# Kernel optimization log

Hardware: AMD Instinct MI355X
Metric: run time of the kernel (lower is better)

The kernel has to match this reference:

```python
import jax, jax.numpy as jnp
import numpy as np

B, N, D, K = 16, 1024, 512, 8
NUM_ITERS = 3
EPS = 1e-08
LN_EPS = 1e-05


def layer_norm(x, g, b):
    m = jnp.mean(x, axis=-1, keepdims=True)
    v = jnp.var(x, axis=-1, keepdims=True)
    return (x - m) * jax.lax.rsqrt(v + LN_EPS) * g + b


def setup_inputs() -> dict:
    key = jax.random.key(0)
    ks = jax.random.split(key, 8)
    s = 1.0 / np.sqrt(D)
    return {
        "embeddings": jax.random.normal(ks[0], (B, N, D), jnp.float32),
        "noise_init": jax.random.normal(ks[1], (B, K, D), jnp.float32),
        "noise_final": jax.random.normal(ks[2], (B, K, D), jnp.float32),
        "slots_mu": jax.random.normal(ks[3], (1, K, D), jnp.float32) * s,
        "slots_logsigma": jax.random.normal(ks[4], (1, K, D), jnp.float32) * s,
        "mixing_coeffs": jnp.ones((1, K), jnp.float32) / K,
        "Wk": jax.random.normal(ks[5], (D, D), jnp.float32) * s,
        "bk": jnp.zeros((D,), jnp.float32),
        "Wq": jax.random.normal(ks[6], (D, D), jnp.float32) * s,
        "bq": jnp.zeros((D,), jnp.float32),
        "Wv": jax.random.normal(ks[7], (D, D), jnp.float32) * s,
        "bv": jnp.zeros((D,), jnp.float32),
        "ln_g": jnp.ones((D,), jnp.float32),
        "ln_b": jnp.zeros((D,), jnp.float32),
    }


def reference(embeddings, noise_init, noise_final, slots_mu, slots_logsigma,
              mixing_coeffs, Wk, bk, Wq, bq, Wv, bv, ln_g, ln_b):
    b, n, d = embeddings.shape
    mixing = jnp.broadcast_to(mixing_coeffs, (b, K))           # [B,K]
    mu = jnp.broadcast_to(slots_mu, (b, K, d))                 # [B,K,D]
    sigma = jnp.exp(jnp.broadcast_to(slots_logsigma, (b, K, d)))
    slots = mu + sigma * noise_init                            # sampled slots

    x = layer_norm(embeddings, ln_g, ln_b)
    keys = x @ Wk + bk                                         # [B,N,D]
    values = x @ Wv + bv                                       # [B,N,D]
    # slots are never updated inside the loop, so queries are loop-invariant
    queries = slots @ Wq + bq                                  # [B,K,D]

    log2pi = jnp.float32(np.log(2.0 * np.pi))
    attn = None
    for _ in range(NUM_ITERS):
        diff = keys[:, :, None, :] - queries[:, None, :, :]    # [B,N,K,D]
        gll = -0.5 * jnp.sum(diff * diff / (sigma[:, None] ** 2 + EPS), axis=-1)  # [B,N,K]
        gll = (-0.5 * d * log2pi
               - 0.5 * jnp.sum(jnp.log(jnp.abs(sigma) + EPS), axis=-1)[:, None, :]
               + gll)
        attn = mixing[:, None, :] * gll                        # [B,N,K]
        attn = attn / jnp.sum(attn, axis=-1, keepdims=True)
        attn = attn / (jnp.sum(attn, axis=1, keepdims=True) + EPS)
        mu = jnp.einsum('bnk,bnd->bkd', attn, values)          # [B,K,D]
        diff2 = values[:, :, None, :] - mu[:, None, :, :]      # [B,N,K,D]
        sigma = jnp.einsum('bnk,bnkd->bkd', attn, diff2 * diff2)
        mixing = jnp.sum(attn, axis=1) / n

    sigma = jnp.maximum(jnp.abs(sigma), EPS)
    slots = mu + sigma * noise_final
    return slots, jnp.transpose(attn, (0, 2, 1))
```

## Files before the change

kernel.cpp:

```cpp
#include <hip/hip_runtime.h>
#include <math.h>

#define BB 16
#define NN 1024
#define DD 512
#define KK 8
#define EPS_ 1e-8f
#define LN_EPS_ 1e-5f
#define GLL_C0 (-470.4965290007924f)

typedef __attribute__((ext_vector_type(8))) short short8;
typedef __attribute__((ext_vector_type(4))) short short4v;
typedef __attribute__((ext_vector_type(4))) float f32x4;
typedef __attribute__((ext_vector_type(4))) int int4v;

static __device__ inline short f2bf(float f) {
    unsigned u = __builtin_bit_cast(unsigned, f);
    u = (u + 0x7fff + ((u >> 16) & 1)) >> 16;
    return (short)u;
}
static __device__ inline float bf2f(short s) {
    unsigned u = ((unsigned)(unsigned short)s) << 16;
    return __builtin_bit_cast(float, u);
}

struct Params {
    const float *emb, *noise_init, *noise_final, *slots_mu, *slots_logsg,
                *mixing_co, *Wk, *bk, *Wq, *bq, *Wv, *bv, *ln_g, *ln_b;
    float *out;
    float *queries, *attn, *s1p, *s2p, *off, *mix16, *colsum;
    short *Abf, *Kbf, *Vbf, *WtKV, *WqT, *slotbf, *F_bt;
};

__global__ __launch_bounds__(256) void k_pre(Params p)
{
    __shared__ __align__(16) short eb[4352];
    int u = blockIdx.x, tid = threadIdx.x;
    if (u < 4096) {
        int row  = u * 4 + (tid >> 6);
        int lane = tid & 63;
        const float* e = p.emb + (size_t)row * DD + lane * 8;
        float4 v0 = *(const float4*)e;
        float4 v1 = *(const float4*)(e + 4);
        float v[8] = {v0.x, v0.y, v0.z, v0.w, v1.x, v1.y, v1.z, v1.w};
        float s = 0.0f;
#pragma unroll
        for (int j = 0; j < 8; j++) s += v[j];
#pragma unroll
        for (int off = 32; off; off >>= 1) s += __shfl_xor(s, off);
        float m = s * (1.0f / DD);
        float vs = 0.0f;
#pragma unroll
        for (int j = 0; j < 8; j++) { float d = v[j] - m; vs = fmaf(d, d, vs); }
#pragma unroll
        for (int off = 32; off; off >>= 1) vs += __shfl_xor(vs, off);
        float rstd = rsqrtf(vs * (1.0f / DD) + LN_EPS_);

        float4 g0 = *(const float4*)&p.ln_g[lane * 8];
        float4 g1 = *(const float4*)&p.ln_g[lane * 8 + 4];
        float4 b0 = *(const float4*)&p.ln_b[lane * 8];
        float4 b1 = *(const float4*)&p.ln_b[lane * 8 + 4];
        float g[8] = {g0.x, g0.y, g0.z, g0.w, g1.x, g1.y, g1.z, g1.w};
        float bb[8] = {b0.x, b0.y, b0.z, b0.w, b1.x, b1.y, b1.z, b1.w};
        short8 o;
#pragma unroll
        for (int j = 0; j < 8; j++) o[j] = f2bf(fmaf((v[j] - m) * rstd, g[j], bb[j]));
        *(short8*)&p.Abf[(size_t)row * DD + lane * 8] = o;
    } else if (u < 4864) {
        int idx = u - 4096;
        int z = idx >> 8, rem = idx & 255;
        const float* W = (z == 0) ? p.Wk : (z == 1) ? p.Wv : p.Wq;
        short* T; int nbase;
        if (z < 2) { T = p.WtKV; nbase = z * 512; } else { T = p.WqT; nbase = 0; }
        int k0 = (rem & 15) * 32, n0 = (rem >> 4) * 32;
        int tx = tid & 31, ty = tid >> 5;
        float (*t)[33] = (float (*)[33])eb;
#pragma unroll
        for (int q = 0; q < 4; q++)
            t[ty + q * 8][tx] = W[(size_t)(k0 + ty + q * 8) * DD + n0 + tx];
        __syncthreads();
#pragma unroll
        for (int q = 0; q < 4; q++)
            T[(size_t)(nbase + n0 + ty + q * 8) * DD + k0 + tx] = f2bf(t[tx][ty + q * 8]);
    } else {
        int idx = u - 4864;
        int b = idx >> 3, k = idx & 7;
#pragma unroll
        for (int q = 0; q < 2; q++) {
            int d = tid + q * 256;
            float sg = expf(p.slots_logsg[k * DD + d]);
            float sl = fmaf(sg, p.noise_init[((size_t)(b * KK + k)) * DD + d],
                            p.slots_mu[k * DD + d]);
            p.slotbf[((size_t)(b * KK + k)) * DD + d] = f2bf(sl);
        }
    }
}

__global__ __launch_bounds__(256) void k_gemm(Params p)
{
    __shared__ __align__(16) short smem[32768];
    int u = blockIdx.x, tid = threadIdx.x;
    int w = tid >> 6, l = tid & 63;
    int x, by, qmode;
    if (u >= 1024) { qmode = 1; x = u - 1024; if (x >= 4) return; by = 128; }
    else           { qmode = 0; x = u >> 7;   by = u & 127; }
    const short* A  = qmode ? p.slotbf : p.Abf + (size_t)by * 128 * DD;
    const short* Bt = qmode ? p.WqT : p.WtKV;
    int row0 = qmode ? 0 : by * 128;
    int col0 = x * 128;

    int sr = l >> 3;
    int sg_off = ((l & 7) ^ sr) * 8;
    int mq = (w & 1) * 64, nq = (w >> 1) * 64;
    int fr = l & 15;
    int orow = (l >> 4) * 4, ocol = l & 15;

    int4v ra[4], rb4[4];
    auto LOADR = [&](int k0) {
#pragma unroll
        for (int j = 0; j < 4; j++) {
            int rbj = w * 32 + j * 8;
            int r   = rbj + sr;
            ra[j]  = *(const int4v*)(A  + (size_t)r * DD + k0 + sg_off);
            rb4[j] = *(const int4v*)(Bt + (size_t)(col0 + r) * DD + k0 + sg_off);
        }
    };
    auto WRITES = [&](int buf) {
        short* As_ = smem + buf * 8192;
        short* Bs_ = smem + 16384 + buf * 8192;
#pragma unroll
        for (int j = 0; j < 4; j++) {
            int rbj = w * 32 + j * 8;
            *(int4v*)&As_[rbj * 64 + l * 8] = ra[j];
            *(int4v*)&Bs_[rbj * 64 + l * 8] = rb4[j];
        }
    };

    f32x4 acc[4][4] = {};
    LOADR(0);
    WRITES(0);
    __syncthreads();
    for (int i = 0; i < 8; i++) {
        if (i < 7) LOADR((i + 1) * 64);
        const short* As_ = smem + (i & 1) * 8192;
        const short* Bs_ = smem + 16384 + (i & 1) * 8192;
#pragma unroll
        for (int kk = 0; kk < 2; kk++) {
            int g = kk * 4 + (l >> 4);
            short8 af[4], bfv[4];
#pragma unroll
            for (int mi = 0; mi < 4; mi++)
                af[mi] = *(const short8*)&As_[(mq + mi * 16 + fr) * 64 + (g ^ (fr & 7)) * 8];
#pragma unroll
            for (int ni = 0; ni < 4; ni++)
                bfv[ni] = *(const short8*)&Bs_[(nq + ni * 16 + fr) * 64 + (g ^ (fr & 7)) * 8];
#pragma unroll
            for (int mi = 0; mi < 4; mi++)
#pragma unroll
                for (int ni = 0; ni < 4; ni++)
                    acc[mi][ni] = __builtin_amdgcn_mfma_f32_16x16x32_bf16(
                        af[mi], bfv[ni], acc[mi][ni], 0, 0, 0);
        }
        if (i < 7) WRITES((i + 1) & 1);
        __syncthreads();
    }

    float bvv[4];
#pragma unroll
    for (int ni = 0; ni < 4; ni++) {
        int col = col0 + nq + ni * 16 + ocol;
        bvv[ni] = qmode ? p.bq[col] : (x < 4 ? p.bk[col] : p.bv[col - 512]);
    }

    if (qmode) {
#pragma unroll
        for (int ni = 0; ni < 4; ni++) {
            int col = col0 + nq + ni * 16 + ocol;
#pragma unroll
            for (int mi = 0; mi < 4; mi++)
#pragma unroll
                for (int r = 0; r < 4; r++)
                    p.queries[(size_t)(mq + mi * 16 + orow + r) * DD + col] =
                        acc[mi][ni][r] + bvv[ni];
        }
    } else {
        short* eb = smem;
        short* dst = (x < 4) ? p.Kbf : p.Vbf;
        int ccol0 = (x & 3) * 128;
#pragma unroll
        for (int mi = 0; mi < 4; mi++)
#pragma unroll
            for (int r = 0; r < 4; r++) {
                int row = mq + mi * 16 + orow + r;
                int sw = ((row >> 2) & 3) << 1;
#pragma unroll
                for (int ni = 0; ni < 4; ni++) {
                    int colg = nq + ni * 16 + ocol;
                    eb[row * 128 + (((colg >> 3) ^ sw) * 8) + (colg & 7)] =
                        f2bf(acc[mi][ni][r] + bvv[ni]);
                }
            }
        __syncthreads();
#pragma unroll
        for (int i = 0; i < 8; i++) {
            int row = i * 16 + w * 4 + (l >> 4);
            int c = l & 15;
            int cc = c ^ (((row >> 2) & 3) << 1);
            short8 vv = *(const short8*)&eb[row * 128 + cc * 8];
            *(short8*)&dst[(size_t)(row0 + row) * 512 + ccol0 + c * 8] = vv;
        }
    }
}

__global__ __launch_bounds__(256) void k_fprep0(Params p)
{
    __shared__ float red[512];
    int u = blockIdx.x, tid = threadIdx.x;
    int b = u >> 4, k = u & 15;
    short* Fr = p.F_bt + (size_t)(b * 16 + k) * 1024;
    if (k >= KK) {
        short4v zv = {0, 0, 0, 0};
        *(short4v*)&Fr[tid * 4] = zv;
        if (tid == 0) { p.off[b * 16 + k] = 0.0f; p.mix16[b * 16 + k] = 0.0f; }
        return;
    }
    float* rc = red;
    float* rl = red + 256;
    float c = 0.0f, ld = 0.0f;
#pragma unroll
    for (int q = 0; q < 2; q++) {
        int d = tid * 2 + q;
        float sg = expf(p.slots_logsg[k * DD + d]);
        float iv = 1.0f / (sg * sg + EPS_);
        float qv = p.queries[((size_t)(b * KK + k)) * DD + d];
        Fr[d]       = f2bf(-0.5f * iv);
        Fr[512 + d] = f2bf(qv * iv);
        c  = fmaf(qv * qv, iv, c);
        ld += logf(fabsf(sg) + EPS_);
    }
    rc[tid] = c; rl[tid] = ld;
    __syncthreads();
    for (int s = 128; s > 0; s >>= 1) {
        if (tid < s) { rc[tid] += rc[tid + s]; rl[tid] += rl[tid + s]; }
        __syncthreads();
    }
    if (tid == 0) {
        p.off[b * 16 + k]    = GLL_C0 - 0.5f * rl[0] - 0.5f * rc[0];
        p.mix16[b * 16 + k]  = p.mixing_co[k];
        p.colsum[b * KK + k] = 0.0f;
    }
}

__global__ __launch_bounds__(512) void k_gllmu(Params p)
{
    __shared__ f32x4 red[3][2][64];
    __shared__ float asml[32 * KK];
    int u = blockIdx.x, tid = threadIdx.x;
    int w = tid >> 6, l = tid & 63;
    int b = u >> 5, chunk = u & 31;
    int n0 = chunk * 32;
    int t = w & 1, ks = w >> 1;

    const short* Ka = p.Kbf + ((size_t)(b * NN + n0 + t * 16 + (l & 15))) * 512
                      + ks * 128 + (l >> 4) * 8;
    const short* Fi = p.F_bt + (size_t)(b * 16 + (l & 15)) * 1024
                      + ks * 128 + (l >> 4) * 8;
    f32x4 acc0 = {}, acc1 = {};
#pragma unroll
    for (int j = 0; j < 4; j++) {
        short8 kf = *(const short8*)&Ka[j * 32];
        short8 f0 = *(const short8*)&Fi[j * 32];
        short8 f1 = *(const short8*)&Fi[j * 32 + 512];
        short8 k2;
#pragma unroll
        for (int e = 0; e < 8; e++) {
            float kv = bf2f(kf[e]);
            k2[e] = f2bf(kv * kv);
        }
        acc0 = __builtin_amdgcn_mfma_f32_16x16x32_bf16(k2, f0, acc0, 0, 0, 0);
        acc1 = __builtin_amdgcn_mfma_f32_16x16x32_bf16(kf, f1, acc1, 0, 0, 0);
    }
    f32x4 acc = acc0 + acc1;

    if (ks) red[ks - 1][t][l] = acc;
    __syncthreads();
    if (ks == 0) {
#pragma unroll
        for (int i = 0; i < 3; i++) acc += red[i][t][l];
        int col = l & 15;
        int rloc = t * 16 + (l >> 4) * 4;
        float offv = p.off[b * 16 + col];
        float mixv = p.mix16[b * 16 + col];
        float a[4], den[4];
#pragma unroll
        for (int r = 0; r < 4; r++) {
            a[r] = mixv * (acc[r] + offv);
            den[r] = a[r];
        }
#pragma unroll
        for (int mask = 1; mask <= 8; mask <<= 1)
#pragma unroll
            for (int r = 0; r < 4; r++) den[r] += __shfl_xor(den[r], mask);
        float csl = 0.0f;
        if (col < KK) {
#pragma unroll
            for (int r = 0; r < 4; r++) {
                float vv = a[r] / den[r];
                asml[(rloc + r) * KK + col] = vv;
                p.attn[((size_t)(b * NN + n0 + rloc + r)) * KK + col] = vv;
                csl += vv;
            }
        }
        csl += __shfl_xor(csl, 16);
        csl += __shfl_xor(csl, 32);
        if (l < KK) atomicAdd(&p.colsum[b * KK + l], csl);
    }
    __syncthreads();

    float s1[KK] = {}, s2[KK] = {};
    const short* vb = p.Vbf + ((size_t)(b * NN + n0)) * DD + tid;
#pragma unroll 4
    for (int nn = 0; nn < 32; nn++) {
        float v = bf2f(vb[(size_t)nn * DD]);
        float vq = v * v;
        float4 a0 = *(const float4*)&asml[nn * KK];
        float4 a1 = *(const float4*)&asml[nn * KK + 4];
        float aa[8] = {a0.x, a0.y, a0.z, a0.w, a1.x, a1.y, a1.z, a1.w};
#pragma unroll
        for (int k = 0; k < KK; k++) {
            s1[k] = fmaf(aa[k], v, s1[k]);
            s2[k] = fmaf(aa[k], vq, s2[k]);
        }
    }
    size_t base = ((size_t)(b * 32 + chunk) * KK) * DD + tid;
#pragma unroll
    for (int k = 0; k < KK; k++) {
        p.s1p[base + (size_t)k * DD] = s1[k];
        p.s2p[base + (size_t)k * DD] = s2[k];
    }
}

__global__ __launch_bounds__(256) void k_fprep(Params p)
{
    __shared__ float red[512];
    int u = blockIdx.x, tid = threadIdx.x;
    int b = u >> 3, k = u & 7;
    float cs   = p.colsum[b * KK + k];
    float inv  = 1.0f / (cs + EPS_);
    float ssum = cs * inv;
    short* Fr = p.F_bt + (size_t)(b * 16 + k) * 1024;
    float* rc = red;
    float* rl = red + 256;
    float c = 0.0f, ld = 0.0f;
#pragma unroll
    for (int q = 0; q < 2; q++) {
        int d = tid * 2 + q;
        float s1 = 0.0f, s2 = 0.0f;
#pragma unroll
        for (int ns = 0; ns < 32; ns++) {
            size_t o = ((size_t)(b * 32 + ns) * KK + k) * DD + d;
            s1 += p.s1p[o];
            s2 += p.s2p[o];
        }
        float m  = s1 * inv;
        float sg = s2 * inv - m * m * (2.0f - ssum);
        float iv = 1.0f / (sg * sg + EPS_);
        float qv = p.queries[((size_t)(b * KK + k)) * DD + d];
        Fr[d]       = f2bf(-0.5f * iv);
        Fr[512 + d] = f2bf(qv * iv);
        c  = fmaf(qv * qv, iv, c);
        ld += logf(fabsf(sg) + EPS_);
    }
    rc[tid] = c; rl[tid] = ld;
    __syncthreads();
    for (int s = 128; s > 0; s >>= 1) {
        if (tid < s) { rc[tid] += rc[tid + s]; rl[tid] += rl[tid + s]; }
        __syncthreads();
    }
    if (tid == 0) {
        p.off[b * 16 + k]    = GLL_C0 - 0.5f * rl[0] - 0.5f * rc[0];
        p.mix16[b * 16 + k]  = ssum * (1.0f / NN);
        p.colsum[b * KK + k] = 0.0f;
    }
}

__global__ __launch_bounds__(256) void k_final(Params p)
{
    int u = blockIdx.x, tid = threadIdx.x;
    if (u < 256) {
        int gid = u * 256 + tid;
        int d = gid & 511;
        int k = (gid >> 9) & 7;
        int b = gid >> 12;
        float s1 = 0.0f, s2 = 0.0f;
#pragma unroll
        for (int ns = 0; ns < 32; ns++) {
            size_t o = ((size_t)(b * 32 + ns) * KK + k) * DD + d;
            s1 += p.s1p[o];
            s2 += p.s2p[o];
        }
        float cs   = p.colsum[b * KK + k];
        float inv  = 1.0f / (cs + EPS_);
        float ssum = cs * inv;
        float m    = s1 * inv;
        float sg   = s2 * inv - m * m * (2.0f - ssum);
        p.out[gid] = fmaf(fmaxf(fabsf(sg), EPS_), p.noise_final[gid], m);
    } else {
        int gid = (u - 256) * 256 + tid;
        int b = gid >> 13;
        int k = (gid >> 10) & 7;
        int n = gid & 1023;
        float cs = p.colsum[b * KK + k];
        p.out[BB * KK * DD + gid] =
            p.attn[((size_t)(b * NN + n)) * KK + k] / (cs + EPS_);
    }
}

extern "C" void kernel_launch(void* const* d_in, const int* in_sizes, int n_in,
                              void* d_out, int out_size, void* d_ws, size_t ws_size,
                              hipStream_t stream)
{
    Params pp;
    pp.emb         = (const float*)d_in[0];
    pp.noise_init  = (const float*)d_in[1];
    pp.noise_final = (const float*)d_in[2];
    pp.slots_mu    = (const float*)d_in[3];
    pp.slots_logsg = (const float*)d_in[4];
    pp.mixing_co   = (const float*)d_in[5];
    pp.Wk          = (const float*)d_in[6];
    pp.bk          = (const float*)d_in[7];
    pp.Wq          = (const float*)d_in[8];
    pp.bq          = (const float*)d_in[9];
    pp.Wv          = (const float*)d_in[10];
    pp.bv          = (const float*)d_in[11];
    pp.ln_g        = (const float*)d_in[12];
    pp.ln_b        = (const float*)d_in[13];
    pp.out         = (float*)d_out;

    float* ws = (float*)d_ws;
    pp.queries = ws;
    pp.attn    = pp.queries + BB * KK * DD;
    pp.s1p     = pp.attn + BB * NN * KK;
    pp.s2p     = pp.s1p + (size_t)BB * 32 * KK * DD;
    pp.off     = pp.s2p + (size_t)BB * 32 * KK * DD;
    pp.mix16   = pp.off + BB * 16;
    pp.colsum  = pp.mix16 + BB * 16;
    pp.Abf     = (short*)(pp.colsum + BB * KK);
    pp.Kbf     = pp.Abf + (size_t)BB * NN * DD;
    pp.Vbf     = pp.Kbf + (size_t)BB * NN * DD;
    pp.WtKV    = pp.Vbf + (size_t)BB * NN * DD;
    pp.WqT     = pp.WtKV + (size_t)1024 * DD;
    pp.slotbf  = pp.WqT + (size_t)DD * DD;
    pp.F_bt    = pp.slotbf + (size_t)BB * KK * DD;

    k_pre<<<4992, 256, 0, stream>>>(pp);
    k_gemm<<<1032, 256, 0, stream>>>(pp);
    k_fprep0<<<256, 256, 0, stream>>>(pp);
    for (int it = 0; it < 3; it++) {
        k_gllmu<<<512, 512, 0, stream>>>(pp);
        if (it < 2) k_fprep<<<128, 256, 0, stream>>>(pp);
    }
    k_final<<<768, 256, 0, stream>>>(pp);
}
```

Baseline: 204.4 us.

## Fuse EM iteration kernels into one cooperative kernel with grid syncs

```diff
diff --git a/kernel.cpp b/kernel.cpp
--- a/kernel.cpp
+++ b/kernel.cpp
@@ -1,5 +1,8 @@
 #include <hip/hip_runtime.h>
+#include <hip/hip_cooperative_groups.h>
 #include <math.h>
+
+namespace cg = cooperative_groups;
 
 #define BB 16
 #define NN 1024
@@ -212,207 +215,204 @@
     }
 }
 
-__global__ __launch_bounds__(256) void k_fprep0(Params p)
+__global__ __launch_bounds__(512, 2) void k_fused(Params p)
 {
-    __shared__ float red[512];
+    __shared__ __align__(16) short ldsV[64][512];
+    __shared__ f32x4 red[4][64];
+    __shared__ __align__(16) float asml[64 * KK];
+    __shared__ float fredc[8], fredl[8];
+
+    cg::grid_group grd = cg::this_grid();
+
     int u = blockIdx.x, tid = threadIdx.x;
-    int b = u >> 4, k = u & 15;
-    short* Fr = p.F_bt + (size_t)(b * 16 + k) * 1024;
-    if (k >= KK) {
-        short4v zv = {0, 0, 0, 0};
-        *(short4v*)&Fr[tid * 4] = zv;
-        if (tid == 0) { p.off[b * 16 + k] = 0.0f; p.mix16[b * 16 + k] = 0.0f; }
-        return;
-    }
-    float* rc = red;
-    float* rl = red + 256;
-    float c = 0.0f, ld = 0.0f;
-#pragma unroll
-    for (int q = 0; q < 2; q++) {
-        int d = tid * 2 + q;
-        float sg = expf(p.slots_logsg[k * DD + d]);
+    int w = tid >> 6, l = tid & 63;
+    int b = u >> 4, cpair = u & 15;
+    int n0 = cpair * 64;
+    int t = w & 3, ks2 = w >> 2;
+
+    {
+        int r0 = (tid >> 6) * 8;
+        int c0 = (tid & 63) * 8;
+        const short* vsrc = p.Vbf + ((size_t)(b * NN + n0)) * DD + c0;
+#pragma unroll
+        for (int i = 0; i < 8; i++)
+            *(short8*)&ldsV[r0 + i][c0] = *(const short8*)&vsrc[(size_t)(r0 + i) * DD];
+    }
+
+    short8 kf[8], k2[8];
+    {
+        const short* Ka = p.Kbf + ((size_t)(b * NN + n0 + t * 16 + (l & 15))) * DD
+                          + ks2 * 256 + (l >> 4) * 8;
+#pragma unroll
+        for (int j = 0; j < 8; j++) {
+            kf[j] = *(const short8*)&Ka[j * 32];
+#pragma unroll
+            for (int e = 0; e < 8; e++) {
+                float kv = bf2f(kf[j][e]);
+                k2[j][e] = f2bf(kv * kv);
+            }
+        }
+    }
+
+    if (u < 128) {
+        int fb = u >> 3, fk = u & 7, d = tid;
+        short* Fr = p.F_bt + (size_t)(fb * 16 + fk) * 1024;
+        float sg = expf(p.slots_logsg[fk * DD + d]);
         float iv = 1.0f / (sg * sg + EPS_);
-        float qv = p.queries[((size_t)(b * KK + k)) * DD + d];
+        float qv = p.queries[((size_t)(fb * KK + fk)) * DD + d];
         Fr[d]       = f2bf(-0.5f * iv);
         Fr[512 + d] = f2bf(qv * iv);
-        c  = fmaf(qv * qv, iv, c);
-        ld += logf(fabsf(sg) + EPS_);
-    }
-    rc[tid] = c; rl[tid] = ld;
-    __syncthreads();
-    for (int s = 128; s > 0; s >>= 1) {
-        if (tid < s) { rc[tid] += rc[tid + s]; rl[tid] += rl[tid + s]; }
-        __syncthreads();
-    }
-    if (tid == 0) {
-        p.off[b * 16 + k]    = GLL_C0 - 0.5f * rl[0] - 0.5f * rc[0];
-        p.mix16[b * 16 + k]  = p.mixing_co[k];
-        p.colsum[b * KK + k] = 0.0f;
-    }
-}
-
-__global__ __launch_bounds__(512) void k_gllmu(Params p)
-{
-    __shared__ f32x4 red[3][2][64];
-    __shared__ float asml[32 * KK];
-    int u = blockIdx.x, tid = threadIdx.x;
-    int w = tid >> 6, l = tid & 63;
-    int b = u >> 5, chunk = u & 31;
-    int n0 = chunk * 32;
-    int t = w & 1, ks = w >> 1;
-
-    const short* Ka = p.Kbf + ((size_t)(b * NN + n0 + t * 16 + (l & 15))) * 512
-                      + ks * 128 + (l >> 4) * 8;
-    const short* Fi = p.F_bt + (size_t)(b * 16 + (l & 15)) * 1024
-                      + ks * 128 + (l >> 4) * 8;
-    f32x4 acc0 = {}, acc1 = {};
-#pragma unroll
-    for (int j = 0; j < 4; j++) {
-        short8 kf = *(const short8*)&Ka[j * 32];
-        short8 f0 = *(const short8*)&Fi[j * 32];
-        short8 f1 = *(const short8*)&Fi[j * 32 + 512];
-        short8 k2;
-#pragma unroll
-        for (int e = 0; e < 8; e++) {
-            float kv = bf2f(kf[e]);
-            k2[e] = f2bf(kv * kv);
-        }
-        acc0 = __builtin_amdgcn_mfma_f32_16x16x32_bf16(k2, f0, acc0, 0, 0, 0);
-        acc1 = __builtin_amdgcn_mfma_f32_16x16x32_bf16(kf, f1, acc1, 0, 0, 0);
-    }
-    f32x4 acc = acc0 + acc1;
-
-    if (ks) red[ks - 1][t][l] = acc;
-    __syncthreads();
-    if (ks == 0) {
-#pragma unroll
-        for (int i = 0; i < 3; i++) acc += red[i][t][l];
-        int col = l & 15;
-        int rloc = t * 16 + (l >> 4) * 4;
-        float offv = p.off[b * 16 + col];
-        float mixv = p.mix16[b * 16 + col];
-        float a[4], den[4];
-#pragma unroll
-        for (int r = 0; r < 4; r++) {
-            a[r] = mixv * (acc[r] + offv);
-            den[r] = a[r];
-        }
-#pragma unroll
-        for (int mask = 1; mask <= 8; mask <<= 1)
-#pragma unroll
-            for (int r = 0; r < 4; r++) den[r] += __shfl_xor(den[r], mask);
-        float csl = 0.0f;
-        if (col < KK) {
-#pragma unroll
-            for (int r = 0; r < 4; r++) {
-                float vv = a[r] / den[r];
-                asml[(rloc + r) * KK + col] = vv;
-                p.attn[((size_t)(b * NN + n0 + rloc + r)) * KK + col] = vv;
-                csl += vv;
-            }
-        }
-        csl += __shfl_xor(csl, 16);
-        csl += __shfl_xor(csl, 32);
-        if (l < KK) atomicAdd(&p.colsum[b * KK + l], csl);
-    }
-    __syncthreads();
-
-    float s1[KK] = {}, s2[KK] = {};
-    const short* vb = p.Vbf + ((size_t)(b * NN + n0)) * DD + tid;
+        float c  = qv * qv * iv;
+        float ld = logf(fabsf(sg) + EPS_);
+#pragma unroll
+        for (int m_ = 32; m_; m_ >>= 1) { c += __shfl_xor(c, m_); ld += __shfl_xor(ld, m_); }
+        if (l == 0) { fredc[w] = c; fredl[w] = ld; }
+        __syncthreads();
+        if (tid == 0) {
+            float rc = 0.0f, rl = 0.0f;
+#pragma unroll
+            for (int i = 0; i < 8; i++) { rc += fredc[i]; rl += fredl[i]; }
+            p.off[fb * 16 + fk]    = GLL_C0 - 0.5f * rl - 0.5f * rc;
+            p.mix16[fb * 16 + fk]  = p.mixing_co[fk];
+            p.colsum[fb * KK + fk] = 0.0f;
+        }
+    } else {
+        int ub = u - 128;
+        int fb = ub >> 3, fk = 8 + (ub & 7);
+        short* Fr = p.F_bt + (size_t)(fb * 16 + fk) * 1024;
+        Fr[tid] = 0; Fr[512 + tid] = 0;
+        if (tid == 0) { p.off[fb * 16 + fk] = 0.0f; p.mix16[fb * 16 + fk] = 0.0f; }
+    }
+    grd.sync();
+
+    for (int it = 0; it < 3; it++) {
+        const short* Fi = p.F_bt + (size_t)(b * 16 + (l & 15)) * 1024
+                          + ks2 * 256 + (l >> 4) * 8;
+        f32x4 acc0 = {}, acc1 = {};
+#pragma unroll
+        for (int j = 0; j < 8; j++) {
+            short8 f0 = *(const short8*)&Fi[j * 32];
+            short8 f1 = *(const short8*)&Fi[j * 32 + 512];
+            acc0 = __builtin_amdgcn_mfma_f32_16x16x32_bf16(k2[j], f0, acc0, 0, 0, 0);
+            acc1 = __builtin_amdgcn_mfma_f32_16x16x32_bf16(kf[j], f1, acc1, 0, 0, 0);
+        }
+        f32x4 acc = acc0 + acc1;
+        if (ks2) red[t][l] = acc;
+        __syncthreads();
+        if (ks2 == 0) {
+            acc += red[t][l];
+            int col = l & 15;
+            int rloc = t * 16 + (l >> 4) * 4;
+            float offv = p.off[b * 16 + col];
+            float mixv = p.mix16[b * 16 + col];
+            float a[4], den[4];
+#pragma unroll
+            for (int r = 0; r < 4; r++) { a[r] = mixv * (acc[r] + offv); den[r] = a[r]; }
+#pragma unroll
+            for (int mask = 1; mask <= 8; mask <<= 1)
+#pragma unroll
+                for (int r = 0; r < 4; r++) den[r] += __shfl_xor(den[r], mask);
+            float csl = 0.0f;
+            if (col < KK) {
+#pragma unroll
+                for (int r = 0; r < 4; r++) {
+                    float vv = a[r] / den[r];
+                    asml[(rloc + r) * KK + col] = vv;
+                    csl += vv;
+                }
+            }
+            csl += __shfl_xor(csl, 16);
+            csl += __shfl_xor(csl, 32);
+            if (l < KK) atomicAdd(&p.colsum[b * KK + l], csl);
+        }
+        __syncthreads();
+
+        float s1[KK] = {}, s2[KK] = {};
 #pragma unroll 4
-    for (int nn = 0; nn < 32; nn++) {
-        float v = bf2f(vb[(size_t)nn * DD]);
-        float vq = v * v;
-        float4 a0 = *(const float4*)&asml[nn * KK];
-        float4 a1 = *(const float4*)&asml[nn * KK + 4];
-        float aa[8] = {a0.x, a0.y, a0.z, a0.w, a1.x, a1.y, a1.z, a1.w};
-#pragma unroll
-        for (int k = 0; k < KK; k++) {
-            s1[k] = fmaf(aa[k], v, s1[k]);
-            s2[k] = fmaf(aa[k], vq, s2[k]);
-        }
-    }
-    size_t base = ((size_t)(b * 32 + chunk) * KK) * DD + tid;
-#pragma unroll
-    for (int k = 0; k < KK; k++) {
-        p.s1p[base + (size_t)k * DD] = s1[k];
-        p.s2p[base + (size_t)k * DD] = s2[k];
-    }
-}
-
-__global__ __launch_bounds__(256) void k_fprep(Params p)
-{
-    __shared__ float red[512];
-    int u = blockIdx.x, tid = threadIdx.x;
-    int b = u >> 3, k = u & 7;
-    float cs   = p.colsum[b * KK + k];
-    float inv  = 1.0f / (cs + EPS_);
-    float ssum = cs * inv;
-    short* Fr = p.F_bt + (size_t)(b * 16 + k) * 1024;
-    float* rc = red;
-    float* rl = red + 256;
-    float c = 0.0f, ld = 0.0f;
-#pragma unroll
-    for (int q = 0; q < 2; q++) {
-        int d = tid * 2 + q;
-        float s1 = 0.0f, s2 = 0.0f;
-#pragma unroll
-        for (int ns = 0; ns < 32; ns++) {
-            size_t o = ((size_t)(b * 32 + ns) * KK + k) * DD + d;
-            s1 += p.s1p[o];
-            s2 += p.s2p[o];
-        }
-        float m  = s1 * inv;
-        float sg = s2 * inv - m * m * (2.0f - ssum);
-        float iv = 1.0f / (sg * sg + EPS_);
-        float qv = p.queries[((size_t)(b * KK + k)) * DD + d];
-        Fr[d]       = f2bf(-0.5f * iv);
-        Fr[512 + d] = f2bf(qv * iv);
-        c  = fmaf(qv * qv, iv, c);
-        ld += logf(fabsf(sg) + EPS_);
-    }
-    rc[tid] = c; rl[tid] = ld;
-    __syncthreads();
-    for (int s = 128; s > 0; s >>= 1) {
-        if (tid < s) { rc[tid] += rc[tid + s]; rl[tid] += rl[tid + s]; }
-        __syncthreads();
-    }
-    if (tid == 0) {
-        p.off[b * 16 + k]    = GLL_C0 - 0.5f * rl[0] - 0.5f * rc[0];
-        p.mix16[b * 16 + k]  = ssum * (1.0f / NN);
-        p.colsum[b * KK + k] = 0.0f;
-    }
-}
-
-__global__ __launch_bounds__(256) void k_final(Params p)
-{
-    int u = blockIdx.x, tid = threadIdx.x;
-    if (u < 256) {
-        int gid = u * 256 + tid;
-        int d = gid & 511;
-        int k = (gid >> 9) & 7;
-        int b = gid >> 12;
-        float s1 = 0.0f, s2 = 0.0f;
-#pragma unroll
-        for (int ns = 0; ns < 32; ns++) {
-            size_t o = ((size_t)(b * 32 + ns) * KK + k) * DD + d;
-            s1 += p.s1p[o];
-            s2 += p.s2p[o];
-        }
-        float cs   = p.colsum[b * KK + k];
+        for (int nn = 0; nn < 64; nn++) {
+            float v  = bf2f(ldsV[nn][tid]);
+            float vq = v * v;
+            float4 a0 = *(const float4*)&asml[nn * KK];
+            float4 a1 = *(const float4*)&asml[nn * KK + 4];
+            float aa[8] = {a0.x, a0.y, a0.z, a0.w, a1.x, a1.y, a1.z, a1.w};
+#pragma unroll
+            for (int k = 0; k < KK; k++) {
+                s1[k] = fmaf(aa[k], v,  s1[k]);
+                s2[k] = fmaf(aa[k], vq, s2[k]);
+            }
+        }
+        {
+            size_t base = ((size_t)((b * 16 + cpair) * KK)) * DD + tid;
+#pragma unroll
+            for (int k = 0; k < KK; k++) {
+                p.s1p[base + (size_t)k * DD] = s1[k];
+                p.s2p[base + (size_t)k * DD] = s2[k];
+            }
+        }
+        grd.sync();
+
+        if (it < 2) {
+            if (u < 128) {
+                int fb = u >> 3, fk = u & 7, d = tid;
+                float s1v = 0.0f, s2v = 0.0f;
+#pragma unroll
+                for (int ns = 0; ns < 16; ns++) {
+                    size_t o = ((size_t)(fb * 16 + ns) * KK + fk) * DD + d;
+                    s1v += p.s1p[o];
+                    s2v += p.s2p[o];
+                }
+                float cs   = p.colsum[fb * KK + fk];
+                float inv  = 1.0f / (cs + EPS_);
+                float ssum = cs * inv;
+                float m  = s1v * inv;
+                float sg = s2v * inv - m * m * (2.0f - ssum);
+                float iv = 1.0f / (sg * sg + EPS_);
+                float qv = p.queries[((size_t)(fb * KK + fk)) * DD + d];
+                short* Fr = p.F_bt + (size_t)(fb * 16 + fk) * 1024;
+                Fr[d]       = f2bf(-0.5f * iv);
+                Fr[512 + d] = f2bf(qv * iv);
+                float c  = qv * qv * iv;
+                float ld = logf(fabsf(sg) + EPS_);
+#pragma unroll
+                for (int m_ = 32; m_; m_ >>= 1) { c += __shfl_xor(c, m_); ld += __shfl_xor(ld, m_); }
+                if (l == 0) { fredc[w] = c; fredl[w] = ld; }
+                __syncthreads();
+                if (tid == 0) {
+                    float rc = 0.0f, rl = 0.0f;
+#pragma unroll
+                    for (int i = 0; i < 8; i++) { rc += fredc[i]; rl += fredl[i]; }
+                    p.off[fb * 16 + fk]    = GLL_C0 - 0.5f * rl - 0.5f * rc;
+                    p.mix16[fb * 16 + fk]  = ssum * (1.0f / NN);
+                    p.colsum[fb * KK + fk] = 0.0f;
+                }
+            }
+            grd.sync();
+        }
+    }
+
+    if (u < 128) {
+        int fb = u >> 3, fk = u & 7, d = tid;
+        float s1v = 0.0f, s2v = 0.0f;
+#pragma unroll
+        for (int ns = 0; ns < 16; ns++) {
+            size_t o = ((size_t)(fb * 16 + ns) * KK + fk) * DD + d;
+            s1v += p.s1p[o];
+            s2v += p.s2p[o];
+        }
+        float cs   = p.colsum[fb * KK + fk];
         float inv  = 1.0f / (cs + EPS_);
         float ssum = cs * inv;
-        float m    = s1 * inv;
-        float sg   = s2 * inv - m * m * (2.0f - ssum);
+        float m    = s1v * inv;
+        float sg   = s2v * inv - m * m * (2.0f - ssum);
+        size_t gid = (size_t)(fb * KK + fk) * DD + d;
         p.out[gid] = fmaf(fmaxf(fabsf(sg), EPS_), p.noise_final[gid], m);
-    } else {
-        int gid = (u - 256) * 256 + tid;
-        int b = gid >> 13;
-        int k = (gid >> 10) & 7;
-        int n = gid & 1023;
-        float cs = p.colsum[b * KK + k];
-        p.out[BB * KK * DD + gid] =
-            p.attn[((size_t)(b * NN + n)) * KK + k] / (cs + EPS_);
+    }
+    {
+        int k  = tid >> 6;
+        int nn = tid & 63;
+        float invcs = 1.0f / (p.colsum[b * KK + k] + EPS_);
+        p.out[(size_t)BB * KK * DD + ((size_t)b * KK + k) * NN + n0 + nn] =
+            asml[nn * KK + k] * invcs;
     }
 }
 
@@ -455,10 +455,6 @@
 
     k_pre<<<4992, 256, 0, stream>>>(pp);
     k_gemm<<<1032, 256, 0, stream>>>(pp);
-    k_fprep0<<<256, 256, 0, stream>>>(pp);
-    for (int it = 0; it < 3; it++) {
-        k_gllmu<<<512, 512, 0, stream>>>(pp);
-        if (it < 2) k_fprep<<<128, 256, 0, stream>>>(pp);
-    }
-    k_final<<<768, 256, 0, stream>>>(pp);
-}
+    void* kargs[] = { (void*)&pp };
+    hipLaunchCooperativeKernel((void*)k_fused, dim3(256), dim3(512), kargs, 0, stream);
+}
```

Measured after the change: 393.3 us. 1.92x slower.

## Load GEMM tiles directly into LDS and skip intermediate attention stores

Applied to the files above, without the earlier changes.

```diff
diff --git a/kernel.cpp b/kernel.cpp
--- a/kernel.cpp
+++ b/kernel.cpp
@@ -115,33 +115,31 @@
     int fr = l & 15;
     int orow = (l >> 4) * 4, ocol = l & 15;
 
-    int4v ra[4], rb4[4];
-    auto LOADR = [&](int k0) {
+    auto STAGE = [&](int k0, int buf) {
+        short* As_ = smem + buf * 8192;
+        short* Bs_ = smem + 16384 + buf * 8192;
 #pragma unroll
         for (int j = 0; j < 4; j++) {
             int rbj = w * 32 + j * 8;
             int r   = rbj + sr;
-            ra[j]  = *(const int4v*)(A  + (size_t)r * DD + k0 + sg_off);
-            rb4[j] = *(const int4v*)(Bt + (size_t)(col0 + r) * DD + k0 + sg_off);
+            __builtin_amdgcn_global_load_lds(
+                (const __attribute__((address_space(1))) unsigned int*)
+                    (A + (size_t)r * DD + k0 + sg_off),
+                (__attribute__((address_space(3))) unsigned int*)
+                    &As_[rbj * 64 + l * 8], 16, 0, 0);
+            __builtin_amdgcn_global_load_lds(
+                (const __attribute__((address_space(1))) unsigned int*)
+                    (Bt + (size_t)(col0 + r) * DD + k0 + sg_off),
+                (__attribute__((address_space(3))) unsigned int*)
+                    &Bs_[rbj * 64 + l * 8], 16, 0, 0);
         }
     };
-    auto WRITES = [&](int buf) {
-        short* As_ = smem + buf * 8192;
-        short* Bs_ = smem + 16384 + buf * 8192;
-#pragma unroll
-        for (int j = 0; j < 4; j++) {
-            int rbj = w * 32 + j * 8;
-            *(int4v*)&As_[rbj * 64 + l * 8] = ra[j];
-            *(int4v*)&Bs_[rbj * 64 + l * 8] = rb4[j];
-        }
-    };
 
     f32x4 acc[4][4] = {};
-    LOADR(0);
-    WRITES(0);
+    STAGE(0, 0);
     __syncthreads();
     for (int i = 0; i < 8; i++) {
-        if (i < 7) LOADR((i + 1) * 64);
+        if (i < 7) STAGE((i + 1) * 64, (i + 1) & 1);
         const short* As_ = smem + (i & 1) * 8192;
         const short* Bs_ = smem + 16384 + (i & 1) * 8192;
 #pragma unroll
@@ -161,7 +159,6 @@
                     acc[mi][ni] = __builtin_amdgcn_mfma_f32_16x16x32_bf16(
                         af[mi], bfv[ni], acc[mi][ni], 0, 0, 0);
         }
-        if (i < 7) WRITES((i + 1) & 1);
         __syncthreads();
     }
 
@@ -251,7 +248,7 @@
     }
 }
 
-__global__ __launch_bounds__(512) void k_gllmu(Params p)
+__global__ __launch_bounds__(512) void k_gllmu(Params p, int itlast)
 {
     __shared__ f32x4 red[3][2][64];
     __shared__ float asml[32 * KK];
@@ -307,7 +304,8 @@
             for (int r = 0; r < 4; r++) {
                 float vv = a[r] / den[r];
                 asml[(rloc + r) * KK + col] = vv;
-                p.attn[((size_t)(b * NN + n0 + rloc + r)) * KK + col] = vv;
+                if (itlast)
+                    p.attn[((size_t)(b * NN + n0 + rloc + r)) * KK + col] = vv;
                 csl += vv;
             }
         }
@@ -457,7 +455,7 @@
     k_gemm<<<1032, 256, 0, stream>>>(pp);
     k_fprep0<<<256, 256, 0, stream>>>(pp);
     for (int it = 0; it < 3; it++) {
-        k_gllmu<<<512, 512, 0, stream>>>(pp);
+        k_gllmu<<<512, 512, 0, stream>>>(pp, it == 2);
         if (it < 2) k_fprep<<<128, 256, 0, stream>>>(pp);
     }
     k_final<<<768, 256, 0, stream>>>(pp);
```

Result: faster. 196.0 us (median of 2 runs) (-4.1%).
